# Optimization experiments

Measured on AMD Instinct MI355X. Metric: run time of the kernel, lower is better.

Reference implementation:

```python
import jax, jax.numpy as jnp
import numpy as np

DN = ('NCHW', 'OIHW', 'NCHW')
THRESHOLD = 20   # Broyden iterations (hardcoded in the torch forward)


def conv(x, k):
    return jax.lax.conv_general_dilated(x, k, (1, 1), 'SAME', dimension_numbers=DN)


def _matvec(Us, VTs, v):
    # (-I + Us @ VTs) v ; Us [B,D,K], VTs [B,K,D], v [B,D]
    return -v + jnp.einsum('bdk,bk->bd', Us, jnp.einsum('bkd,bd->bk', VTs, v))


def _rmatvec(Us, VTs, v):
    # v^T (-I + Us @ VTs)
    return -v + jnp.einsum('bk,bkd->bd', jnp.einsum('bd,bdk->bk', v, Us), VTs)


def broyden_solve(g, x0, threshold):
    """Broyden's method with low-rank inverse-Jacobian updates (J^{-1} = -I + Us VTs),
    returning the iterate with the lowest residual norm (as in the DEQ broyden solver)."""
    B, D = x0.shape
    x, gx = x0, g(x0)
    Us = jnp.zeros((B, D, threshold), x0.dtype)
    VTs = jnp.zeros((B, threshold, D), x0.dtype)
    best_x, best_obj = x, jnp.linalg.norm(gx)
    update = gx  # -(-I) gx with empty low-rank part
    for k in range(threshold):
        x_new = x + update
        gx_new = g(x_new)
        dx, dgx = x_new - x, gx_new - gx
        vT = _rmatvec(Us, VTs, dx)                       # [B,D]
        denom = jnp.einsum('bd,bd->b', vT, dgx)[:, None]
        denom = jnp.where(jnp.abs(denom) < 1e-9, 1e-9, denom)
        u = (dx - _matvec(Us, VTs, dgx)) / denom
        Us = Us.at[:, :, k].set(u)
        VTs = VTs.at[:, k, :].set(vT)
        x, gx = x_new, gx_new
        obj = jnp.linalg.norm(gx)
        best_x = jnp.where(obj < best_obj, x, best_x)
        best_obj = jnp.minimum(obj, best_obj)
        update = -_matvec(Us, VTs, gx)
    return best_x


def setup_inputs() -> dict:
    key = jax.random.key(0)
    k1, k2, k3, k4 = jax.random.split(key, 4)
    B, Cin, Cout, H, W = 16, 64, 128, 32, 32
    x = jax.random.normal(k1, (B, Cin, H, W), jnp.float32)
    # small-norm A so relu(conv(z,A)+...) is a contraction -> equilibrium exists
    A = jax.random.normal(k2, (Cout, Cout, 3, 3), jnp.float32) * 0.02
    U = jax.random.normal(k3, (Cout, Cin, 3, 3), jnp.float32) * 0.05
    b = jax.random.normal(k4, (1, Cout, 1, 1), jnp.float32) * 0.1
    return {'x': x, 'A': A, 'U': U, 'b': b}


def reference(x, A, U, b):
    B, _, H, W = x.shape
    Cout = A.shape[0]
    D = Cout * H * W
    ux = conv(x, U) + b  # input injection, constant over iterations

    def g(zvec):  # residual g(z) = relu(Wz + Ux + b) - z, flattened
        z = zvec.reshape(B, Cout, H, W)
        return (jax.nn.relu(conv(z, A) + ux) - z).reshape(B, D)

    z0 = jnp.zeros((B, D), x.dtype)
    zstar = broyden_solve(g, z0, THRESHOLD).reshape(B, Cout, H, W)
    # final recompute with the equilibrium (the torch code re-runs linear+nonlin)
    zn = jax.nn.relu(conv(zstar, A) + ux)
    return zn
```

## Files before the change

kernel.cpp:

```cpp
#include <hip/hip_runtime.h>

#define NB    16
#define CIN_  64
#define COUT_ 128
#define PLANE_ 1024
#define DDIM  (COUT_*PLANE_)
#define BDTOT ((size_t)NB*DDIM)
#define KMAX  20
#define SMAX  16
#define SEG   (DDIM / SMAX)
#define GRP8  (SEG / 8)
#define CBLK  128
#define PADC  8

typedef short  bfrag __attribute__((ext_vector_type(8)));
typedef float  ffrag __attribute__((ext_vector_type(4)));

__device__ __forceinline__ float bf2f(unsigned short h) {
    return __uint_as_float(((unsigned int)h) << 16);
}
__device__ __forceinline__ unsigned short f2bf(float f) {
    unsigned int u = __float_as_uint(f);
    u = (u + 0x7FFFu + ((u >> 16) & 1u)) >> 16;
    return (unsigned short)u;
}
__device__ __forceinline__ void bf2x(unsigned int w, float& lo, float& hi) {
    lo = __uint_as_float(w << 16);
    hi = __uint_as_float(w & 0xffff0000u);
}
__device__ __forceinline__ unsigned int packbf(float lo, float hi) {
    return ((unsigned int)f2bf(hi) << 16) | (unsigned int)f2bf(lo);
}
__device__ __forceinline__ void ub4(ushort4 a, float* f) {
    f[0] = bf2f(a.x); f[1] = bf2f(a.y); f[2] = bf2f(a.z); f[3] = bf2f(a.w);
}
__device__ __forceinline__ ushort4 pk4(const float* f) {
    ushort4 r; r.x = f2bf(f[0]); r.y = f2bf(f[1]); r.z = f2bf(f[2]); r.w = f2bf(f[3]);
    return r;
}
__device__ __forceinline__ void ub8(uint4 a, float* f) {
    bf2x(a.x, f[0], f[1]); bf2x(a.y, f[2], f[3]);
    bf2x(a.z, f[4], f[5]); bf2x(a.w, f[6], f[7]);
}
__device__ __forceinline__ float wred(float v) {
    #pragma unroll
    for (int m = 32; m > 0; m >>= 1) v += __shfl_xor(v, m, 64);
    return v;
}

template<int CIN>
__device__ __forceinline__ void conv_stage_lds(
    const unsigned short* __restrict__ zsrc, unsigned short* lds,
    int hrow, int n, int tid)
{
    const int CP = CIN + PADC;
    const int CH8 = CIN / 8;
    for (int idx = tid; idx < 102 * CH8; idx += 256) {
        int slot = idx / CH8, chunk = idx - slot * CH8;
        int row = slot / 34, pxm = slot - row * 34;
        int h = hrow + row - 1, w = pxm - 1;
        uint4 val = {0u, 0u, 0u, 0u};
        if ((unsigned)h < 32u && (unsigned)w < 32u)
            val = *(const uint4*)(zsrc + ((size_t)n * PLANE_ + h * 32 + w) * CIN + chunk * 8);
        *(uint4*)(lds + (slot)*CP + chunk * 8) = val;
    }
    __syncthreads();
}

template<int CIN>
__device__ __forceinline__ void conv_compute_lds(
    const unsigned short* lds, const unsigned short* __restrict__ Wt,
    int co_base, int col, int quad, ffrag accs[4])
{
    const int CP = CIN + PADC;
    #pragma unroll
    for (int cb = 0; cb < CIN; cb += 32) {
        #pragma unroll
        for (int tap = 0; tap < 9; ++tap) {
            const int dh = tap / 3, dwi = tap % 3;
            const unsigned short* wr0 =
                Wt + ((size_t)tap * COUT_ + co_base + col) * CIN + quad * 8 + cb;
            bfrag a0 = *(const bfrag*)(wr0);
            bfrag a1 = *(const bfrag*)(wr0 + 16 * CIN);
            bfrag b0 = *(const bfrag*)(lds + (dh * 34 + col + dwi) * CP + cb + quad * 8);
            bfrag b1 = *(const bfrag*)(lds + (dh * 34 + col + 16 + dwi) * CP + cb + quad * 8);
            accs[0] = __builtin_amdgcn_mfma_f32_16x16x32_bf16(a0, b0, accs[0], 0, 0, 0);
            accs[1] = __builtin_amdgcn_mfma_f32_16x16x32_bf16(a0, b1, accs[1], 0, 0, 0);
            accs[2] = __builtin_amdgcn_mfma_f32_16x16x32_bf16(a1, b0, accs[2], 0, 0, 0);
            accs[3] = __builtin_amdgcn_mfma_f32_16x16x32_bf16(a1, b1, accs[3], 0, 0, 0);
        }
    }
}

__global__ __launch_bounds__(256) void conv_ux_kernel(
    const unsigned short* __restrict__ xinb, const unsigned short* __restrict__ WU,
    const float* __restrict__ bias, float* __restrict__ ux,
    unsigned short* __restrict__ uxb)
{
    __shared__ unsigned short lds[3 * 34 * (CIN_ + PADC)];
    const int hrow = blockIdx.x, n = blockIdx.y;
    const int tid = threadIdx.x, lane = tid & 63, wv = tid >> 6;
    const int col = lane & 15, quad = lane >> 4;
    conv_stage_lds<CIN_>(xinb, lds, hrow, n, tid);
    ffrag accs[4] = {{0.f,0.f,0.f,0.f},{0.f,0.f,0.f,0.f},{0.f,0.f,0.f,0.f},{0.f,0.f,0.f,0.f}};
    conv_compute_lds<CIN_>(lds, WU, wv * 32, col, quad, accs);
    #pragma unroll
    for (int f = 0; f < 4; ++f) {
        const int mt = f >> 1, nt = f & 1;
        const int co = wv * 32 + mt * 16 + quad * 4;
        const int px = hrow * 32 + nt * 16 + col;
        const size_t o = ((size_t)n * PLANE_ + px) * COUT_ + co;
        float4 bv = *(const float4*)(bias + co);
        float r[4] = {accs[f][0] + bv.x, accs[f][1] + bv.y, accs[f][2] + bv.z, accs[f][3] + bv.w};
        *(float4*)(ux + o) = make_float4(r[0], r[1], r[2], r[3]);
        *(ushort4*)(uxb + o) = pk4(r);
    }
}

__global__ __launch_bounds__(256) void conv_bro_kernel(
    const unsigned short* __restrict__ zb, const unsigned short* __restrict__ WA,
    const unsigned short* __restrict__ uxb, const float* __restrict__ xv,
    unsigned short* gxb,
    const unsigned short* __restrict__ updb,
    unsigned short* __restrict__ dgxb,
    float* __restrict__ cparts)
{
    __shared__ unsigned short lds[3 * 34 * (COUT_ + PADC)];
    const int hrow = blockIdx.x, n = blockIdx.y;
    const int tid = threadIdx.x, lane = tid & 63, wv = tid >> 6;
    const int col = lane & 15, quad = lane >> 4;
    conv_stage_lds<COUT_>(zb, lds, hrow, n, tid);
    ffrag accs[4] = {{0.f,0.f,0.f,0.f},{0.f,0.f,0.f,0.f},{0.f,0.f,0.f,0.f},{0.f,0.f,0.f,0.f}};
    conv_compute_lds<COUT_>(lds, WA, wv * 32, col, quad, accs);

    float s0 = 0.f, s1 = 0.f, s2 = 0.f, s3 = 0.f, s4 = 0.f, s5 = 0.f;
    #pragma unroll
    for (int f = 0; f < 4; ++f) {
        const int mt = f >> 1, nt = f & 1;
        const int co = wv * 32 + mt * 16 + quad * 4;
        const int px = hrow * 32 + nt * 16 + col;
        const size_t o = ((size_t)n * PLANE_ + px) * COUT_ + co;
        float uxv[4], gov[4], udv[4];
        ub4(*(const ushort4*)(uxb + o), uxv);
        ub4(*(const ushort4*)(gxb + o), gov);
        ub4(*(const ushort4*)(updb + o), udv);
        float4 xc = *(const float4*)(xv + o);
        float g[4], dgv[4];
        #pragma unroll
        for (int r = 0; r < 4; ++r) {
            float tv = accs[f][r] + uxv[r];
            tv = tv > 0.f ? tv : 0.f;
            g[r] = tv - (&xc.x)[r];
            dgv[r] = g[r] - gov[r];
            s0 += udv[r] * dgv[r];
            s1 += udv[r] * g[r];
            s2 += g[r] * g[r];
            s3 += udv[r] * udv[r];
            s4 += dgv[r] * dgv[r];
            s5 += dgv[r] * g[r];
        }
        *(ushort4*)(gxb + o)  = pk4(g);
        *(ushort4*)(dgxb + o) = pk4(dgv);
    }
    s0 = wred(s0); s1 = wred(s1); s2 = wred(s2);
    s3 = wred(s3); s4 = wred(s4); s5 = wred(s5);
    if (lane == 0) {
        const int blk = hrow * 4 + wv;
        cparts[((size_t)0 * NB + n) * CBLK + blk] = s0;
        cparts[((size_t)1 * NB + n) * CBLK + blk] = s1;
        cparts[((size_t)2 * NB + n) * CBLK + blk] = s2;
        cparts[((size_t)3 * NB + n) * CBLK + blk] = s3;
        cparts[((size_t)4 * NB + n) * CBLK + blk] = s4;
        cparts[((size_t)5 * NB + n) * CBLK + blk] = s5;
    }
}

__global__ __launch_bounds__(256) void conv_final_kernel(
    const unsigned short* __restrict__ bestzb, const unsigned short* __restrict__ WA,
    const float* __restrict__ ux, float* __restrict__ out)
{
    __shared__ unsigned short lds[3 * 34 * (COUT_ + PADC)];
    const int hrow = blockIdx.x, n = blockIdx.y;
    const int tid = threadIdx.x, lane = tid & 63, wv = tid >> 6;
    const int col = lane & 15, quad = lane >> 4;
    conv_stage_lds<COUT_>(bestzb, lds, hrow, n, tid);
    ffrag accs[4] = {{0.f,0.f,0.f,0.f},{0.f,0.f,0.f,0.f},{0.f,0.f,0.f,0.f},{0.f,0.f,0.f,0.f}};
    conv_compute_lds<COUT_>(lds, WA, wv * 32, col, quad, accs);
    #pragma unroll
    for (int f = 0; f < 4; ++f) {
        const int mt = f >> 1, nt = f & 1;
        const int co = wv * 32 + mt * 16 + quad * 4;
        const int px = hrow * 32 + nt * 16 + col;
        const size_t o = ((size_t)n * PLANE_ + px) * COUT_ + co;
        float4 uv = *(const float4*)(ux + o);
        #pragma unroll
        for (int r = 0; r < 4; ++r) {
            float t = accs[f][r] + (&uv.x)[r];
            out[((size_t)n * COUT_ + co + r) * PLANE_ + px] = t > 0.f ? t : 0.f;
        }
    }
}

#define NWA (9 * 128 * 128)
#define NWU (9 * 128 * 64)
__global__ __launch_bounds__(256) void prep_w_kernel(
    const float* __restrict__ A, const float* __restrict__ U,
    unsigned short* __restrict__ WA, unsigned short* __restrict__ WU)
{
    int idx = blockIdx.x * 256 + threadIdx.x;
    if (idx < NWA) {
        int tap = idx / (128 * 128), r = idx % (128 * 128);
        int co = r >> 7, ci = r & 127;
        WA[idx] = f2bf(A[(co * 128 + ci) * 9 + tap]);
    } else if (idx < NWA + NWU) {
        int j = idx - NWA;
        int tap = j / (128 * 64), r = j % (128 * 64);
        int co = r >> 6, ci = r & 63;
        WU[j] = f2bf(U[(co * 64 + ci) * 9 + tap]);
    }
}

__global__ __launch_bounds__(256) void prep_xin_kernel(
    const float* __restrict__ x, unsigned short* __restrict__ xb)
{
    int idx = blockIdx.x * 256 + threadIdx.x;
    int n = idx >> 16, r = idx & 65535;
    int px = r >> 6, ci = r & 63;
    xb[idx] = f2bf(x[(n * 64 + ci) * 1024 + px]);
}

__global__ __launch_bounds__(256) void fill0_kernel(float* __restrict__ a)
{
    size_t i = ((size_t)blockIdx.x * 256 + threadIdx.x) * 4;
    *(float4*)(a + i) = make_float4(0.f, 0.f, 0.f, 0.f);
}

__global__ __launch_bounds__(256) void ew_init_kernel(
    const float* __restrict__ ux, unsigned short* __restrict__ gxb,
    unsigned short* __restrict__ updb, float* __restrict__ xv,
    unsigned short* __restrict__ zb, float* __restrict__ objinit)
{
    const int tid = threadIdx.x;
    size_t i = ((size_t)blockIdx.x * 256 + tid) * 8;
    float rr[8];
    float ob = 0.f;
    #pragma unroll
    for (int h = 0; h < 2; ++h) {
        float4 u = *(const float4*)(ux + i + h * 4);
        #pragma unroll
        for (int r = 0; r < 4; ++r) {
            float v = (&u.x)[r];
            v = v > 0.f ? v : 0.f;
            v = bf2f(f2bf(v));
            rr[h*4+r] = v;
            ob += v * v;
        }
    }
    uint4 m = {packbf(rr[0],rr[1]), packbf(rr[2],rr[3]), packbf(rr[4],rr[5]), packbf(rr[6],rr[7])};
    *(uint4*)(gxb  + i) = m;
    *(uint4*)(updb + i) = m;
    *(uint4*)(zb   + i) = m;
    #pragma unroll
    for (int h = 0; h < 2; ++h)
        *(float4*)(xv + i + h * 4) = make_float4(rr[h*4+0], rr[h*4+1], rr[h*4+2], rr[h*4+3]);

    __shared__ float so[256];
    so[tid] = ob;
    __syncthreads();
    for (int s = 128; s > 0; s >>= 1) {
        if (tid < s) so[tid] += so[tid + s];
        __syncthreads();
    }
    if (tid == 0) objinit[blockIdx.x] = so[0];
}

__global__ __launch_bounds__(256) void dots_kernel(
    const unsigned short* __restrict__ Us, const unsigned short* __restrict__ VTs,
    const unsigned short* __restrict__ dgxb,
    float* __restrict__ tparts, int k)
{
    const int b = blockIdx.x, y = blockIdx.y, s = blockIdx.z;
    const int tid = threadIdx.x;
    const size_t segbase = (size_t)b * DDIM + (size_t)s * SEG;
    const unsigned short* M = (y < k) ? (VTs + (size_t)y * BDTOT)
                                      : (Us + (size_t)(y - k) * BDTOT);
    const uint4* m8 = (const uint4*)(M + segbase);
    const uint4* d8 = (const uint4*)(dgxb + segbase);
    float s0 = 0.f;
    #pragma unroll
    for (int it = 0; it < GRP8 / 256; ++it) {
        int g = it * 256 + tid;
        float mv[8], dv[8];
        ub8(m8[g], mv); ub8(d8[g], dv);
        #pragma unroll
        for (int j = 0; j < 8; ++j) s0 = fmaf(mv[j], dv[j], s0);
    }
    __shared__ float r0[256];
    r0[tid] = s0;
    __syncthreads();
    for (int st = 128; st > 0; st >>= 1) {
        if (tid < st) r0[tid] += r0[tid + st];
        __syncthreads();
    }
    if (tid == 0) tparts[((size_t)y * NB + b) * SMAX + s] = r0[0];
}

__global__ __launch_bounds__(256) void pass2_kernel(
    unsigned short* __restrict__ Us, unsigned short* __restrict__ VTs,
    unsigned short* updb,
    const unsigned short* __restrict__ dgxb, const unsigned short* __restrict__ gxb,
    float* xv, unsigned short* __restrict__ zb, unsigned short* __restrict__ bestzb,
    const float* __restrict__ tparts, const float* __restrict__ cparts,
    const float* __restrict__ objinit,
    const float* __restrict__ parr_r, float* __restrict__ parr_w,
    const float* __restrict__ tp_r, float* __restrict__ tp_w,
    const float* __restrict__ hp_r, float* __restrict__ hp_w,
    float* __restrict__ UU, float* __restrict__ obj_arr, int k)
{
    const int b = blockIdx.y;
    const int bx = blockIdx.x;
    const int tid = threadIdx.x;
    const int lane = tid & 63, wv = tid >> 6;

    __shared__ float sq[KMAX], st[KMAX], sp[KMAX], sr[KMAX], sh[KMAX], UUk[KMAX];
    __shared__ float sS[5];
    __shared__ float sden, sc, sflag, sobj, srk;
    __shared__ float red[256];

    {
        float o = 0.f;
        const float* OB = cparts + (size_t)2 * NB * CBLK;
        for (int j = tid; j < NB * CBLK; j += 256) o += OB[j];
        red[tid] = o;
        __syncthreads();
        for (int s = 128; s > 0; s >>= 1) {
            if (tid < s) red[tid] += red[tid + s];
            __syncthreads();
        }
        if (tid == 0) sobj = red[0];
        __syncthreads();
    }
    float obj0 = 0.f;
    if (k == 0) {
        float o = 0.f;
        for (int j = tid; j < 1024; j += 256) o += objinit[j];
        red[tid] = o;
        __syncthreads();
        for (int s = 128; s > 0; s >>= 1) {
            if (tid < s) red[tid] += red[tid + s];
            __syncthreads();
        }
        obj0 = red[0];
        __syncthreads();
    }

    if (tid < k) {
        float qv = 0.f, rv = 0.f;
        #pragma unroll
        for (int s = 0; s < SMAX; ++s) {
            qv += tparts[((size_t)tid * NB + b) * SMAX + s];
            rv += tparts[((size_t)(k + tid) * NB + b) * SMAX + s];
        }
        sq[tid] = qv; sr[tid] = rv;
        st[tid] = qv + tp_r[b * KMAX + tid];
        sh[tid] = rv + hp_r[b * KMAX + tid];
        sp[tid] = parr_r[b * KMAX + tid];
    }
    if (wv == 1) {
        float a0 = 0.f, a1 = 0.f;
        for (int j = lane; j < CBLK; j += 64) {
            a0 += cparts[((size_t)0 * NB + b) * CBLK + j];
            a1 += cparts[((size_t)3 * NB + b) * CBLK + j];
        }
        a0 = wred(a0); a1 = wred(a1);
        if (lane == 0) { sS[0] = a0; sS[2] = a1; }
    } else if (wv == 2) {
        float a0 = 0.f, a1 = 0.f;
        for (int j = lane; j < CBLK; j += 64) {
            a0 += cparts[((size_t)1 * NB + b) * CBLK + j];
            a1 += cparts[((size_t)4 * NB + b) * CBLK + j];
        }
        a0 = wred(a0); a1 = wred(a1);
        if (lane == 0) { sS[1] = a0; sS[3] = a1; }
    } else if (wv == 3) {
        float a0 = 0.f;
        for (int j = lane; j < CBLK; j += 64)
            a0 += cparts[((size_t)5 * NB + b) * CBLK + j];
        a0 = wred(a0);
        if (lane == 0) sS[4] = a0;
    }
    __syncthreads();

    if (tid == 0) {
        float pq = 0.f, pt = 0.f;
        for (int i = 0; i < k; ++i) { pq += sp[i] * sq[i]; pt += sp[i] * st[i]; }
        float den = -sS[0] + pq;
        if (fabsf(den) < 1e-9f) den = 1e-9f;
        sden = den;
        float rk = -sS[1] + pt;
        srk = rk;
        sc = rk / den;
        float best;
        if (k == 0) best = obj0;
        else {
            best = obj_arr[0];
            for (int j = 1; j <= k; ++j) best = fminf(best, obj_arr[j]);
        }
        sflag = (sobj < best) ? 1.f : 0.f;
    }
    __syncthreads();

    const size_t base = (size_t)b * DDIM + ((size_t)bx * 256 + tid) * 8;
    float xd[8], dg[8], gv[8];
    ub8(*(const uint4*)(updb + base), xd);
    ub8(*(const uint4*)(dgxb + base), dg);
    ub8(*(const uint4*)(gxb  + base), gv);

    float S1[8], S2[8], SV[8];
    #pragma unroll
    for (int j = 0; j < 8; ++j) { S1[j] = 0.f; S2[j] = 0.f; SV[j] = 0.f; }

    int i = 0;
    for (; i + 1 < k; i += 2) {
        uint4 ru0 = *(const uint4*)(Us  + (size_t)i * BDTOT + base);
        uint4 rv0 = *(const uint4*)(VTs + (size_t)i * BDTOT + base);
        uint4 ru1 = *(const uint4*)(Us  + (size_t)(i + 1) * BDTOT + base);
        uint4 rv1 = *(const uint4*)(VTs + (size_t)(i + 1) * BDTOT + base);
        float u0[8], v0[8], u1[8], v1[8];
        ub8(ru0, u0); ub8(rv0, v0); ub8(ru1, u1); ub8(rv1, v1);
        float q0 = sq[i], t0 = st[i], p0 = sp[i];
        float q1 = sq[i+1], t1 = st[i+1], p1 = sp[i+1];
        #pragma unroll
        for (int j = 0; j < 8; ++j) {
            S1[j] = fmaf(q0, u0[j], fmaf(q1, u1[j], S1[j]));
            S2[j] = fmaf(t0, u0[j], fmaf(t1, u1[j], S2[j]));
            SV[j] = fmaf(p0, v0[j], fmaf(p1, v1[j], SV[j]));
        }
    }
    if (i < k) {
        float uvals[8], vvals[8];
        ub8(*(const uint4*)(Us  + (size_t)i * BDTOT + base), uvals);
        ub8(*(const uint4*)(VTs + (size_t)i * BDTOT + base), vvals);
        float qi = sq[i], ti = st[i], pi = sp[i];
        #pragma unroll
        for (int j = 0; j < 8; ++j) {
            S1[j] = fmaf(qi, uvals[j], S1[j]);
            S2[j] = fmaf(ti, uvals[j], S2[j]);
            SV[j] = fmaf(pi, vvals[j], SV[j]);
        }
    }

    float vk[8], uk[8], up[8];
    #pragma unroll
    for (int j = 0; j < 8; ++j) {
        vk[j] = -xd[j] + SV[j];
        uk[j] = (xd[j] + dg[j] - S1[j]) / sden;
        up[j] = gv[j] - sc * (xd[j] + dg[j]) - S2[j] + sc * S1[j];
    }
    uint4 vks = {packbf(vk[0],vk[1]), packbf(vk[2],vk[3]), packbf(vk[4],vk[5]), packbf(vk[6],vk[7])};
    uint4 uks = {packbf(uk[0],uk[1]), packbf(uk[2],uk[3]), packbf(uk[4],uk[5]), packbf(uk[6],uk[7])};
    *(uint4*)(VTs + (size_t)k * BDTOT + base) = vks;
    *(uint4*)(Us  + (size_t)k * BDTOT + base) = uks;

    uint4 upw = {packbf(up[0],up[1]), packbf(up[2],up[3]), packbf(up[4],up[5]), packbf(up[6],up[7])};
    *(uint4*)(updb + base) = upw;
    float upr[8];
    ub8(upw, upr);

    float xc[8];
    #pragma unroll
    for (int h = 0; h < 2; ++h) {
        float4 a = *(const float4*)(xv + base + h * 4);
        xc[h*4+0]=a.x; xc[h*4+1]=a.y; xc[h*4+2]=a.z; xc[h*4+3]=a.w;
    }
    if (sflag != 0.f) {
        uint4 bz = {packbf(xc[0],xc[1]), packbf(xc[2],xc[3]),
                    packbf(xc[4],xc[5]), packbf(xc[6],xc[7])};
        *(uint4*)(bestzb + base) = bz;
    }
    float xn[8];
    #pragma unroll
    for (int j = 0; j < 8; ++j) xn[j] = xc[j] + upr[j];
    #pragma unroll
    for (int h = 0; h < 2; ++h)
        *(float4*)(xv + base + h * 4) = make_float4(xn[h*4+0], xn[h*4+1], xn[h*4+2], xn[h*4+3]);
    uint4 zn = {packbf(xn[0],xn[1]), packbf(xn[2],xn[3]), packbf(xn[4],xn[5]), packbf(xn[6],xn[7])};
    *(uint4*)(zb + base) = zn;

    if (bx == 0) {
        const float den = sden, cc = sc;
        if (tid < k) {
            float acc = sp[tid] + sr[tid];
            for (int j = 0; j < k; ++j)
                acc -= sq[j] * UU[((size_t)b * KMAX + j) * KMAX + tid];
            UUk[tid] = acc / den;
        }
        __syncthreads();
        if (tid == 0) {
            float ww = sS[2] + 2.f * sS[0] + sS[3];
            float wg = sS[1] + sS[4];
            float sumqh = 0.f, sumqpr = 0.f, sumqU = 0.f;
            for (int j = 0; j < k; ++j) {
                sumqh += sq[j] * sh[j];
                sumqpr += sq[j] * (sp[j] + sr[j]);
                sumqU += sq[j] * UUk[j];
            }
            float ug = (wg - sumqh) / den;
            float uw = (ww - sumqpr) / den;
            float UUkk = (uw - sumqU) / den;
            for (int l = 0; l < k; ++l) {
                UU[((size_t)b * KMAX + k) * KMAX + l] = UUk[l];
                UU[((size_t)b * KMAX + l) * KMAX + k] = UUk[l];
            }
            UU[((size_t)b * KMAX + k) * KMAX + k] = UUkk;
            float acc = ug - cc * uw;
            for (int l = 0; l < k; ++l)
                acc -= (st[l] - cc * sq[l]) * UUk[l];
            parr_w[b * KMAX + k] = acc;
            tp_w[b * KMAX + k] = srk;
            hp_w[b * KMAX + k] = ug;
            if (b == 0) {
                if (k == 0) obj_arr[0] = obj0;
                obj_arr[k + 1] = sobj;
            }
        }
        if (tid < k) {
            float acc = sh[tid] - cc * (sp[tid] + sr[tid]);
            for (int l = 0; l < k; ++l)
                acc -= (st[l] - cc * sq[l]) * UU[((size_t)b * KMAX + tid) * KMAX + l];
            parr_w[b * KMAX + tid] = acc;
            tp_w[b * KMAX + tid] = st[tid];
            hp_w[b * KMAX + tid] = sh[tid];
        }
    }
}

__global__ __launch_bounds__(256) void bestfinal_kernel(
    const float* __restrict__ cparts, const float* __restrict__ obj_arr,
    const unsigned short* __restrict__ zb, unsigned short* __restrict__ bestzb)
{
    const int tid = threadIdx.x;
    __shared__ float red[256];
    __shared__ float sflag;
    float o = 0.f;
    const float* OB = cparts + (size_t)2 * NB * CBLK;
    for (int j = tid; j < NB * CBLK; j += 256) o += OB[j];
    red[tid] = o;
    __syncthreads();
    for (int s = 128; s > 0; s >>= 1) {
        if (tid < s) red[tid] += red[tid + s];
        __syncthreads();
    }
    if (tid == 0) {
        float best = obj_arr[0];
        for (int j = 1; j < KMAX; ++j) best = fminf(best, obj_arr[j]);
        sflag = (red[0] < best) ? 1.f : 0.f;
    }
    __syncthreads();
    if (sflag == 0.f) return;
    size_t i = ((size_t)blockIdx.x * 256 + tid) * 8;
    *(uint4*)(bestzb + i) = *(const uint4*)(zb + i);
}

extern "C" void kernel_launch(void* const* d_in, const int* in_sizes, int n_in,
                              void* d_out, int out_size, void* d_ws, size_t ws_size,
                              hipStream_t stream)
{
    (void)in_sizes; (void)n_in; (void)out_size; (void)ws_size;
    const float* x  = (const float*)d_in[0];
    const float* A  = (const float*)d_in[1];
    const float* U  = (const float*)d_in[2];
    const float* bb = (const float*)d_in[3];
    float* out = (float*)d_out;

    char* w = (char*)d_ws;
    size_t off = 0;
    auto alloc = [&](size_t bytes) -> void* {
        void* pp = (void*)(w + off);
        off += (bytes + 255) & ~(size_t)255;
        return pp;
    };
    const size_t BDB  = BDTOT * sizeof(float);
    const size_t BDH  = BDTOT * 2;
    float* ux    = (float*)alloc(BDB);
    float* xv    = (float*)alloc(BDB);
    unsigned short* uxb    = (unsigned short*)alloc(BDH);
    unsigned short* gxb    = (unsigned short*)alloc(BDH);
    unsigned short* updb   = (unsigned short*)alloc(BDH);
    unsigned short* dgxb   = (unsigned short*)alloc(BDH);
    unsigned short* zb     = (unsigned short*)alloc(BDH);
    unsigned short* bestzb = (unsigned short*)alloc(BDH);
    unsigned short* xinb   = (unsigned short*)alloc((size_t)NB * PLANE_ * CIN_ * 2);
    unsigned short* WA     = (unsigned short*)alloc((size_t)NWA * 2);
    unsigned short* WU     = (unsigned short*)alloc((size_t)NWU * 2);
    unsigned short* Us  = (unsigned short*)alloc((size_t)KMAX * BDTOT * 2);
    unsigned short* VTs = (unsigned short*)alloc((size_t)KMAX * BDTOT * 2);
    float* cparts = (float*)alloc((size_t)6 * NB * CBLK * sizeof(float));
    float* tparts = (float*)alloc((size_t)2 * KMAX * NB * SMAX * sizeof(float));
    float* objinit= (float*)alloc(1024 * sizeof(float));
    float* parr0 = (float*)alloc(NB * KMAX * sizeof(float));
    float* parr1 = (float*)alloc(NB * KMAX * sizeof(float));
    float* tp0   = (float*)alloc(NB * KMAX * sizeof(float));
    float* tp1   = (float*)alloc(NB * KMAX * sizeof(float));
    float* hp0   = (float*)alloc(NB * KMAX * sizeof(float));
    float* hp1   = (float*)alloc(NB * KMAX * sizeof(float));
    float* UU    = (float*)alloc((size_t)NB * KMAX * KMAX * sizeof(float));
    float* obj_arr = (float*)alloc((KMAX + 1) * sizeof(float));

    const dim3 CG(32, NB);
    const int I8WG = (int)(BDTOT / (256 * 8));

    prep_w_kernel<<<(NWA + NWU + 255) / 256, 256, 0, stream>>>(A, U, WA, WU);
    prep_xin_kernel<<<(NB * PLANE_ * CIN_) / 256, 256, 0, stream>>>(x, xinb);
    fill0_kernel<<<(int)(BDH / (256 * 16)), 256, 0, stream>>>((float*)bestzb);

    conv_ux_kernel<<<CG, 256, 0, stream>>>(xinb, WU, bb, ux, uxb);
    ew_init_kernel<<<I8WG, 256, 0, stream>>>(ux, gxb, updb, xv, zb, objinit);

    float* parr[2] = {parr0, parr1};
    float* tp[2]   = {tp0, tp1};
    float* hp[2]   = {hp0, hp1};
    for (int k = 0; k < KMAX; ++k) {
        conv_bro_kernel<<<CG, 256, 0, stream>>>(zb, WA, uxb, xv, gxb, updb, dgxb, cparts);
        if (k < KMAX - 1) {
            if (k > 0)
                dots_kernel<<<dim3(NB, 2 * k, SMAX), 256, 0, stream>>>(
                    Us, VTs, dgxb, tparts, k);
            pass2_kernel<<<dim3(DDIM / 2048, NB), 256, 0, stream>>>(
                Us, VTs, updb, dgxb, gxb, xv, zb, bestzb,
                tparts, cparts, objinit,
                parr[k & 1], parr[(k + 1) & 1],
                tp[k & 1], tp[(k + 1) & 1],
                hp[k & 1], hp[(k + 1) & 1],
                UU, obj_arr, k);
        } else {
            bestfinal_kernel<<<I8WG, 256, 0, stream>>>(cparts, obj_arr, zb, bestzb);
        }
    }

    conv_final_kernel<<<CG, 256, 0, stream>>>(bestzb, WA, ux, out);
}
```

Baseline: 1.348 ms.

## Fuse low-rank dot products into conv kernel, removing separate dots kernel

Moves the per-iteration dot products of dgx against all stored VTs and Us columns into the conv/Broyden epilogue. They are computed from the register-resident dgx values and emitted as per-wave partial sums. pass2 now reduces these 128 partials per vector instead of the old segment partials. This removes one kernel launch and one re-read of dgx per iteration. In exchange, the conv kernel gets a longer tail with strided ushort4 loads of the Us/VTs rows, which may coalesce less well than the old contiguous uint4 streaming.

```diff
diff --git a/kernel.cpp b/kernel.cpp
--- a/kernel.cpp
+++ b/kernel.cpp
@@ -7,9 +7,6 @@
 #define DDIM  (COUT_*PLANE_)
 #define BDTOT ((size_t)NB*DDIM)
 #define KMAX  20
-#define SMAX  16
-#define SEG   (DDIM / SMAX)
-#define GRP8  (SEG / 8)
 #define CBLK  128
 #define PADC  8
 
@@ -46,6 +43,22 @@
     #pragma unroll
     for (int m = 32; m > 0; m >>= 1) v += __shfl_xor(v, m, 64);
     return v;
+}
+
+__device__ __forceinline__ float dot16(const unsigned short* __restrict__ R,
+                                       const float* dg)
+{
+    float a[4];
+    float acc = 0.f;
+    ub4(*(const ushort4*)(R), a);
+    acc = fmaf(a[0], dg[0], fmaf(a[1], dg[1], fmaf(a[2], dg[2], fmaf(a[3], dg[3], acc))));
+    ub4(*(const ushort4*)(R + 16 * COUT_), a);
+    acc = fmaf(a[0], dg[4], fmaf(a[1], dg[5], fmaf(a[2], dg[6], fmaf(a[3], dg[7], acc))));
+    ub4(*(const ushort4*)(R + 16), a);
+    acc = fmaf(a[0], dg[8], fmaf(a[1], dg[9], fmaf(a[2], dg[10], fmaf(a[3], dg[11], acc))));
+    ub4(*(const ushort4*)(R + 16 * COUT_ + 16), a);
+    acc = fmaf(a[0], dg[12], fmaf(a[1], dg[13], fmaf(a[2], dg[14], fmaf(a[3], dg[15], acc))));
+    return acc;
 }
 
 template<int CIN>
@@ -123,7 +136,9 @@
     unsigned short* gxb,
     const unsigned short* __restrict__ updb,
     unsigned short* __restrict__ dgxb,
-    float* __restrict__ cparts)
+    float* __restrict__ cparts,
+    const unsigned short* __restrict__ Us, const unsigned short* __restrict__ VTs,
+    float* __restrict__ qrparts, int kd)
 {
     __shared__ unsigned short lds[3 * 34 * (COUT_ + PADC)];
     const int hrow = blockIdx.x, n = blockIdx.y;
@@ -134,6 +149,7 @@
     conv_compute_lds<COUT_>(lds, WA, wv * 32, col, quad, accs);
 
     float s0 = 0.f, s1 = 0.f, s2 = 0.f, s3 = 0.f, s4 = 0.f, s5 = 0.f;
+    float dgall[16];
     #pragma unroll
     for (int f = 0; f < 4; ++f) {
         const int mt = f >> 1, nt = f & 1;
@@ -160,8 +176,28 @@
             s5 += dgv[r] * g[r];
         }
         *(ushort4*)(gxb + o)  = pk4(g);
-        *(ushort4*)(dgxb + o) = pk4(dgv);
-    }
+        ushort4 dpk = pk4(dgv);
+        *(ushort4*)(dgxb + o) = dpk;
+        ub4(dpk, dgall + f * 4);
+    }
+
+    if (kd > 0) {
+        const size_t o00 = ((size_t)n * PLANE_ + hrow * 32 + col) * COUT_ + wv * 32 + quad * 4;
+        const int blk = hrow * 4 + wv;
+        #pragma unroll 2
+        for (int i = 0; i < kd; ++i) {
+            float acc = dot16(VTs + (size_t)i * BDTOT + o00, dgall);
+            acc = wred(acc);
+            if (lane == 0) qrparts[((size_t)i * NB + n) * CBLK + blk] = acc;
+        }
+        #pragma unroll 2
+        for (int i = 0; i < kd; ++i) {
+            float acc = dot16(Us + (size_t)i * BDTOT + o00, dgall);
+            acc = wred(acc);
+            if (lane == 0) qrparts[((size_t)(kd + i) * NB + n) * CBLK + blk] = acc;
+        }
+    }
+
     s0 = wred(s0); s1 = wred(s1); s2 = wred(s2);
     s3 = wred(s3); s4 = wred(s4); s5 = wred(s5);
     if (lane == 0) {
@@ -274,43 +310,12 @@
     if (tid == 0) objinit[blockIdx.x] = so[0];
 }
 
-__global__ __launch_bounds__(256) void dots_kernel(
-    const unsigned short* __restrict__ Us, const unsigned short* __restrict__ VTs,
-    const unsigned short* __restrict__ dgxb,
-    float* __restrict__ tparts, int k)
-{
-    const int b = blockIdx.x, y = blockIdx.y, s = blockIdx.z;
-    const int tid = threadIdx.x;
-    const size_t segbase = (size_t)b * DDIM + (size_t)s * SEG;
-    const unsigned short* M = (y < k) ? (VTs + (size_t)y * BDTOT)
-                                      : (Us + (size_t)(y - k) * BDTOT);
-    const uint4* m8 = (const uint4*)(M + segbase);
-    const uint4* d8 = (const uint4*)(dgxb + segbase);
-    float s0 = 0.f;
-    #pragma unroll
-    for (int it = 0; it < GRP8 / 256; ++it) {
-        int g = it * 256 + tid;
-        float mv[8], dv[8];
-        ub8(m8[g], mv); ub8(d8[g], dv);
-        #pragma unroll
-        for (int j = 0; j < 8; ++j) s0 = fmaf(mv[j], dv[j], s0);
-    }
-    __shared__ float r0[256];
-    r0[tid] = s0;
-    __syncthreads();
-    for (int st = 128; st > 0; st >>= 1) {
-        if (tid < st) r0[tid] += r0[tid + st];
-        __syncthreads();
-    }
-    if (tid == 0) tparts[((size_t)y * NB + b) * SMAX + s] = r0[0];
-}
-
 __global__ __launch_bounds__(256) void pass2_kernel(
     unsigned short* __restrict__ Us, unsigned short* __restrict__ VTs,
     unsigned short* updb,
     const unsigned short* __restrict__ dgxb, const unsigned short* __restrict__ gxb,
     float* xv, unsigned short* __restrict__ zb, unsigned short* __restrict__ bestzb,
-    const float* __restrict__ tparts, const float* __restrict__ cparts,
+    const float* __restrict__ qrparts, const float* __restrict__ cparts,
     const float* __restrict__ objinit,
     const float* __restrict__ parr_r, float* __restrict__ parr_w,
     const float* __restrict__ tp_r, float* __restrict__ tp_w,
@@ -354,17 +359,15 @@
         __syncthreads();
     }
 
-    if (tid < k) {
-        float qv = 0.f, rv = 0.f;
+    for (int y = wv; y < 2 * k; y += 4) {
+        float a = 0.f;
         #pragma unroll
-        for (int s = 0; s < SMAX; ++s) {
-            qv += tparts[((size_t)tid * NB + b) * SMAX + s];
-            rv += tparts[((size_t)(k + tid) * NB + b) * SMAX + s];
-        }
-        sq[tid] = qv; sr[tid] = rv;
-        st[tid] = qv + tp_r[b * KMAX + tid];
-        sh[tid] = rv + hp_r[b * KMAX + tid];
-        sp[tid] = parr_r[b * KMAX + tid];
+        for (int j = 0; j < CBLK / 64; ++j)
+            a += qrparts[((size_t)y * NB + b) * CBLK + j * 64 + lane];
+        a = wred(a);
+        if (lane == 0) {
+            if (y < k) sq[y] = a; else sr[y - k] = a;
+        }
     }
     if (wv == 1) {
         float a0 = 0.f, a1 = 0.f;
@@ -388,6 +391,13 @@
             a0 += cparts[((size_t)5 * NB + b) * CBLK + j];
         a0 = wred(a0);
         if (lane == 0) sS[4] = a0;
+    }
+    __syncthreads();
+
+    if (tid < k) {
+        st[tid] = sq[tid] + tp_r[b * KMAX + tid];
+        sh[tid] = sr[tid] + hp_r[b * KMAX + tid];
+        sp[tid] = parr_r[b * KMAX + tid];
     }
     __syncthreads();
 
@@ -596,7 +606,7 @@
     unsigned short* Us  = (unsigned short*)alloc((size_t)KMAX * BDTOT * 2);
     unsigned short* VTs = (unsigned short*)alloc((size_t)KMAX * BDTOT * 2);
     float* cparts = (float*)alloc((size_t)6 * NB * CBLK * sizeof(float));
-    float* tparts = (float*)alloc((size_t)2 * KMAX * NB * SMAX * sizeof(float));
+    float* qrparts= (float*)alloc((size_t)2 * KMAX * NB * CBLK * sizeof(float));
     float* objinit= (float*)alloc(1024 * sizeof(float));
     float* parr0 = (float*)alloc(NB * KMAX * sizeof(float));
     float* parr1 = (float*)alloc(NB * KMAX * sizeof(float));
@@ -621,14 +631,13 @@
     float* tp[2]   = {tp0, tp1};
     float* hp[2]   = {hp0, hp1};
     for (int k = 0; k < KMAX; ++k) {
-        conv_bro_kernel<<<CG, 256, 0, stream>>>(zb, WA, uxb, xv, gxb, updb, dgxb, cparts);
+        const int kd = (k < KMAX - 1) ? k : 0;
+        conv_bro_kernel<<<CG, 256, 0, stream>>>(zb, WA, uxb, xv, gxb, updb, dgxb,
+                                                cparts, Us, VTs, qrparts, kd);
         if (k < KMAX - 1) {
-            if (k > 0)
-                dots_kernel<<<dim3(NB, 2 * k, SMAX), 256, 0, stream>>>(
-                    Us, VTs, dgxb, tparts, k);
             pass2_kernel<<<dim3(DDIM / 2048, NB), 256, 0, stream>>>(
                 Us, VTs, updb, dgxb, gxb, xv, zb, bestzb,
-                tparts, cparts, objinit,
+                qrparts, cparts, objinit,
                 parr[k & 1], parr[(k + 1) & 1],
                 tp[k & 1], tp[(k + 1) & 1],
                 hp[k & 1], hp[(k + 1) & 1],
```

Result: slower. 1.450 ms (+7.6%).
